# Performance work log

Hardware: AMD Instinct MI355X
Metric: run time of the kernel (lower is better)

Reference implementation:

```python
import jax, jax.numpy as jnp
import numpy as np

ALPHA = 2
SQUARE_LUT = jnp.arange(16, dtype=jnp.float32) ** 2
INV_SQRT_LUT = jnp.array([65535, 46341, 32768, 23170, 16384, 11585, 8192, 5793,
                          4096, 2896, 2048, 1448, 1024, 724, 512, 362], dtype=jnp.float32)


def setup_inputs() -> dict:
    key = jax.random.key(0)
    kx, = jax.random.split(key, 1)
    B, N = 8192, 4096
    x = jax.random.normal(kx, (B, N), dtype=jnp.float32)
    gamma = jnp.ones((N,), dtype=jnp.float32)
    beta = jnp.zeros((N,), dtype=jnp.float32)
    return {"x": x, "gamma": gamma, "beta": beta}


def _forward(x, gamma, beta):
    N = x.shape[1]
    # input quantization to int8 range (STE irrelevant for fwd)
    scale_in = jnp.max(jnp.abs(x)) / 127.0
    x_int = jnp.clip(jnp.round(x / scale_in), -127.0, 127.0)
    x_q = x_int * scale_in

    Ex = jnp.sum(x_q, axis=1, keepdims=True)

    abs_q = jnp.abs(x_q)
    top2 = jnp.floor(abs_q / 64.0)
    idx_h = jnp.clip(jnp.floor(abs_q / 16.0), 0, 15).astype(jnp.int32)
    idx_m = jnp.clip(jnp.mod(jnp.floor(abs_q / 2.0), 16.0), 0, 15).astype(jnp.int32)
    hi = top2 >= 1
    idx = jnp.where(hi, idx_h, idx_m)
    sq = SQUARE_LUT[idx]
    sq_decomp = jnp.where(hi, sq * 16.0, sq)
    sq_ref = sq_decomp * (2.0 ** (2 * ALPHA))
    Ex2 = jnp.sum(sq_ref, axis=1, keepdims=True)

    mu = Ex / N
    var = Ex2 / N - mu * mu
    var_int = jnp.clip(jnp.round(var), 1.0, 2.0 ** 16 - 1)
    msb = jnp.clip(jnp.floor(jnp.log2(var_int)), 0, 15).astype(jnp.int32)
    inv_std = INV_SQRT_LUT[msb] / (2.0 ** 16)

    x_norm = (x_q - mu) * inv_std
    y = x_norm * gamma + beta

    scale_out = jnp.max(jnp.abs(y)) / 127.0
    y_int = jnp.clip(jnp.round(y / scale_out), -127.0, 127.0)
    return y_int * scale_out


def reference(x, gamma, beta):
    return _forward(x, gamma, beta)
```

## Files before the change

### kernel.cpp

```cpp
#include <hip/hip_runtime.h>
#include <cstdint>
#include <cstddef>

#define NC    4096
#define NTHR  256
#define R4    4
#define NBUCK 256

typedef float v4f __attribute__((ext_vector_type(4)));

static __device__ __forceinline__ float waveReduceMax(float v) {
    #pragma unroll
    for (int off = 32; off > 0; off >>= 1)
        v = fmaxf(v, __shfl_down(v, off, 64));
    return v;
}
static __device__ __forceinline__ float waveReduceSum(float v) {
    #pragma unroll
    for (int off = 32; off > 0; off >>= 1)
        v += __shfl_down(v, off, 64);
    return v;
}

__device__ __forceinline__ float blockMax(float v, float* s4, int tid) {
    v = waveReduceMax(v);
    int lane = tid & 63, wid = tid >> 6;
    if (lane == 0) s4[wid] = v;
    __syncthreads();
    return fmaxf(fmaxf(s4[0], s4[1]), fmaxf(s4[2], s4[3]));
}

__device__ __forceinline__ void rowStatCompute(float Ex, float Ex2,
                                               float* mu_o, float* inv_o) {
    float mu  = Ex * (1.f / NC);
    float var = __fsub_rn(Ex2 * (1.f / NC), __fmul_rn(mu, mu));
    float var_f = fminf(fmaxf(rintf(var), 1.f), 65535.f);
    int vi = (int)var_f;
    int msb = min(31 - __clz(vi), 15);
    const float lut[16] = {65535.f, 46341.f, 32768.f, 23170.f, 16384.f, 11585.f,
                           8192.f, 5793.f, 4096.f, 2896.f, 2048.f, 1448.f,
                           1024.f, 724.f, 512.f, 362.f};
    *mu_o  = mu;
    *inv_o = lut[msb] * (1.f / 65536.f);
}

__global__ __launch_bounds__(NTHR) void k_absmax(const float* __restrict__ x,
                                                 unsigned int* __restrict__ amax_bits,
                                                 int n4) {
    const float4* x4 = (const float4*)x;
    int t = blockIdx.x * NTHR + threadIdx.x;
    int S = gridDim.x * NTHR;
    float m = 0.f;
    int full = (n4 / (S * 8)) * (S * 8);
    for (int base = t; base < full; base += S * 8) {
        float4 v[8];
        #pragma unroll
        for (int u = 0; u < 8; ++u) v[u] = x4[base + u * S];
        #pragma unroll
        for (int u = 0; u < 8; ++u)
            m = fmaxf(m, fmaxf(fmaxf(fabsf(v[u].x), fabsf(v[u].y)),
                               fmaxf(fabsf(v[u].z), fabsf(v[u].w))));
    }
    for (int i = full + t; i < n4; i += S) {
        float4 v = x4[i];
        m = fmaxf(m, fmaxf(fmaxf(fabsf(v.x), fabsf(v.y)),
                           fmaxf(fabsf(v.z), fabsf(v.w))));
    }
    __shared__ float s4[4];
    float b = blockMax(m, s4, threadIdx.x);
    if (threadIdx.x == 0) atomicMax(amax_bits, __float_as_uint(b));
}

__global__ __launch_bounds__(NTHR) void k_rowstats4(
    const float* __restrict__ x,
    const float* __restrict__ gamma,
    const float* __restrict__ beta,
    const unsigned int* __restrict__ amax_x_bits,
    unsigned int* __restrict__ ybuck,
    float2* __restrict__ row_stats,
    int* __restrict__ xi8)
{
    const int tid = threadIdx.x;
    const int base_row = blockIdx.x * R4;
    const float scale_in = __uint_as_float(*amax_x_bits) * (1.0f / 127.0f);
    const float r_in = 1.0f / scale_in;

    const float4* g4 = (const float4*)gamma;
    const float4* b4 = (const float4*)beta;
    float4 gh[4], bh[4];
    #pragma unroll
    for (int k = 0; k < 4; ++k) { gh[k] = g4[tid + k * NTHR]; bh[k] = b4[tid + k * NTHR]; }

    float exr[R4], ex2r[R4];
    int pack[R4][4];
    #pragma unroll
    for (int r = 0; r < R4; ++r) {
        const int row = base_row + r;
        const float4* xr = (const float4*)(x + (size_t)row * NC);
        float4 v[4];
        #pragma unroll
        for (int k = 0; k < 4; ++k) v[k] = xr[tid + k * NTHR];

        float ex = 0.f, ex2 = 0.f;
        #pragma unroll
        for (int k = 0; k < 4; ++k) {
            const float* pv = (const float*)&v[k];
            int pk = 0;
            #pragma unroll
            for (int j = 0; j < 4; ++j) {
                float xi = fminf(fmaxf(rintf(pv[j] * r_in), -127.f), 127.f);
                int ii = (int)xi;
                pk |= (ii & 255) << (8 * j);
                float q = xi * scale_in;
                ex += q;
                float aq = fabsf(q);
                bool hi = aq >= 64.f;
                int idx = hi ? min((int)(aq * 0.0625f), 15)
                             : (((int)(aq * 0.5f)) & 15);
                float sq = (float)(idx * idx);
                ex2 += hi ? sq * 256.f : sq * 16.f;
            }
            pack[r][k] = pk;
        }
        exr[r] = ex; ex2r[r] = ex2;
        int* wr = xi8 + (size_t)row * (NC / 4);
        #pragma unroll
        for (int k = 0; k < 4; ++k) wr[tid + k * NTHR] = pack[r][k];
    }

    #pragma unroll
    for (int r = 0; r < R4; ++r) {
        exr[r]  = waveReduceSum(exr[r]);
        ex2r[r] = waveReduceSum(ex2r[r]);
    }
    __shared__ float sred[4][8];
    __shared__ float2 s_st[R4];
    const int lane = tid & 63, wid = tid >> 6;
    if (lane == 0) {
        #pragma unroll
        for (int r = 0; r < R4; ++r) { sred[wid][r] = exr[r]; sred[wid][4 + r] = ex2r[r]; }
    }
    __syncthreads();
    if (tid < R4) {
        float Ex  = (sred[0][tid] + sred[1][tid]) + (sred[2][tid] + sred[3][tid]);
        float Ex2 = (sred[0][4 + tid] + sred[1][4 + tid]) + (sred[2][4 + tid] + sred[3][4 + tid]);
        float mu, inv;
        rowStatCompute(Ex, Ex2, &mu, &inv);
        s_st[tid] = make_float2(mu, inv);
        row_stats[base_row + tid] = make_float2(mu, inv);
    }
    __syncthreads();

    float ym = 0.f;
    #pragma unroll
    for (int r = 0; r < R4; ++r) {
        const float mu = s_st[r].x, inv = s_st[r].y;
        #pragma unroll
        for (int k = 0; k < 4; ++k) {
            const float* pg = (const float*)&gh[k];
            const float* pb = (const float*)&bh[k];
            int pk = pack[r][k];
            #pragma unroll
            for (int j = 0; j < 4; ++j) {
                int ii = (pk << (24 - 8 * j)) >> 24;
                float q = (float)ii * scale_in;
                float y = (q - mu) * inv * pg[j] + pb[j];
                ym = fmaxf(ym, fabsf(y));
            }
        }
    }
    __shared__ float smax[4];
    float bym = blockMax(ym, smax, tid);
    if (tid == 0) atomicMax(&ybuck[blockIdx.x & (NBUCK - 1)], __float_as_uint(bym));
}

__global__ __launch_bounds__(NTHR) void k_finalize4(
    const int* __restrict__ xi8,
    const float* __restrict__ gamma,
    const float* __restrict__ beta,
    const unsigned int* __restrict__ amax_x_bits,
    const unsigned int* __restrict__ ybuck,
    const float2* __restrict__ row_stats,
    float* __restrict__ out)
{
    const int tid = threadIdx.x;
    const int base_row = blockIdx.x * R4;
    const float scale_in = __uint_as_float(*amax_x_bits) * (1.0f / 127.0f);

    float by = __uint_as_float(ybuck[tid]);
    __shared__ float s4[4];
    float pym = blockMax(by, s4, tid);
    const float scale_out = pym * (1.f / 127.f);
    const float r_out = 1.f / scale_out;

    const float4* g4 = (const float4*)gamma;
    const float4* b4 = (const float4*)beta;
    float4 gh[4], bh[4];
    #pragma unroll
    for (int k = 0; k < 4; ++k) { gh[k] = g4[tid + k * NTHR]; bh[k] = b4[tid + k * NTHR]; }

    #pragma unroll
    for (int r = 0; r < R4; ++r) {
        const int row = base_row + r;
        const int* rd = xi8 + (size_t)row * (NC / 4);
        int pk[4];
        #pragma unroll
        for (int k = 0; k < 4; ++k) pk[k] = rd[tid + k * NTHR];
        const float2 st = row_stats[row];
        const float mu = st.x, inv = st.y;
        float* outr = out + (size_t)row * NC;
        #pragma unroll
        for (int k = 0; k < 4; ++k) {
            const float* pg = (const float*)&gh[k];
            const float* pb = (const float*)&bh[k];
            v4f o;
            #pragma unroll
            for (int j = 0; j < 4; ++j) {
                int ii = (pk[k] << (24 - 8 * j)) >> 24;
                float q = (float)ii * scale_in;
                float y = (q - mu) * inv * pg[j] + pb[j];
                float yi = fminf(fmaxf(rintf(y * r_out), -127.f), 127.f);
                o[j] = yi * scale_out;
            }
            __builtin_nontemporal_store(o, (v4f*)(outr + (tid + k * NTHR) * 4));
        }
    }
}

__global__ __launch_bounds__(256) void k_rowstats_fb(
    const float* __restrict__ x, const float* __restrict__ gamma,
    const float* __restrict__ beta, const unsigned int* __restrict__ amax_x_bits,
    unsigned int* __restrict__ amax_y_bits, float2* __restrict__ row_stats,
    int* __restrict__ xi8)
{
    const int row = blockIdx.x;
    const float scale_in = __uint_as_float(*amax_x_bits) * (1.0f / 127.0f);
    const float r_in = 1.0f / scale_in;
    const float4* xr = (const float4*)(x + (size_t)row * NC);
    const float4* g4 = (const float4*)gamma;
    const float4* b4 = (const float4*)beta;
    int pack[4];
    float ex = 0.f, ex2 = 0.f;
    #pragma unroll
    for (int k = 0; k < 4; ++k) {
        float4 v = xr[threadIdx.x + k * 256];
        const float* pv = (const float*)&v;
        int pk = 0;
        #pragma unroll
        for (int j = 0; j < 4; ++j) {
            float xi = fminf(fmaxf(rintf(pv[j] * r_in), -127.f), 127.f);
            int ii = (int)xi;
            pk |= (ii & 255) << (8 * j);
            float q = xi * scale_in;
            ex += q;
            float aq = fabsf(q);
            bool hi = aq >= 64.f;
            int idx = hi ? min((int)(aq * 0.0625f), 15) : (((int)(aq * 0.5f)) & 15);
            float sq = (float)(idx * idx);
            ex2 += hi ? sq * 256.f : sq * 16.f;
        }
        pack[k] = pk;
    }
    int* wr = xi8 + (size_t)row * (NC / 4);
    #pragma unroll
    for (int k = 0; k < 4; ++k) wr[threadIdx.x + k * 256] = pack[k];
    ex  = waveReduceSum(ex);
    ex2 = waveReduceSum(ex2);
    __shared__ float sred[8];
    __shared__ float sbc[2];
    int lane = threadIdx.x & 63, wid = threadIdx.x >> 6;
    if (lane == 0) { sred[wid] = ex; sred[4 + wid] = ex2; }
    __syncthreads();
    if (threadIdx.x == 0) {
        float Ex  = (sred[0] + sred[1]) + (sred[2] + sred[3]);
        float Ex2 = (sred[4] + sred[5]) + (sred[6] + sred[7]);
        float mu, inv;
        rowStatCompute(Ex, Ex2, &mu, &inv);
        sbc[0] = mu; sbc[1] = inv;
        row_stats[row] = make_float2(mu, inv);
    }
    __syncthreads();
    const float mu = sbc[0], inv = sbc[1];
    float ym = 0.f;
    #pragma unroll
    for (int k = 0; k < 4; ++k) {
        float4 g = g4[threadIdx.x + k * 256];
        float4 b = b4[threadIdx.x + k * 256];
        const float* pg = (const float*)&g;
        const float* pb = (const float*)&b;
        int pk = pack[k];
        #pragma unroll
        for (int j = 0; j < 4; ++j) {
            int ii = (pk << (24 - 8 * j)) >> 24;
            float q = (float)ii * scale_in;
            float y = (q - mu) * inv * pg[j] + pb[j];
            ym = fmaxf(ym, fabsf(y));
        }
    }
    __syncthreads();
    __shared__ float smax[4];
    float b = blockMax(ym, smax, threadIdx.x);
    if (threadIdx.x == 0) atomicMax(amax_y_bits, __float_as_uint(b));
}

__global__ __launch_bounds__(256) void k_finalize_fb(
    const int* __restrict__ xi8, const float* __restrict__ gamma,
    const float* __restrict__ beta, const unsigned int* __restrict__ amax_x_bits,
    const unsigned int* __restrict__ amax_y_bits,
    const float2* __restrict__ row_stats, float* __restrict__ out)
{
    const int row = blockIdx.x;
    const float scale_in  = __uint_as_float(*amax_x_bits) * (1.0f / 127.0f);
    const float scale_out = __uint_as_float(*amax_y_bits) * (1.0f / 127.0f);
    const float r_out = 1.0f / scale_out;
    const float2 st = row_stats[row];
    const float mu = st.x, inv = st.y;
    const int* xr = xi8 + (size_t)row * (NC / 4);
    float4* outr = (float4*)(out + (size_t)row * NC);
    const float4* g4 = (const float4*)gamma;
    const float4* b4 = (const float4*)beta;
    #pragma unroll
    for (int k = 0; k < 4; ++k) {
        int pk = xr[threadIdx.x + k * 256];
        float4 g = g4[threadIdx.x + k * 256];
        float4 b = b4[threadIdx.x + k * 256];
        float4 o;
        const float* pg = (const float*)&g;
        const float* pb = (const float*)&b;
        float* po = (float*)&o;
        #pragma unroll
        for (int j = 0; j < 4; ++j) {
            int ii = (pk << (24 - 8 * j)) >> 24;
            float q = (float)ii * scale_in;
            float y = (q - mu) * inv * pg[j] + pb[j];
            float yi = fminf(fmaxf(rintf(y * r_out), -127.f), 127.f);
            po[j] = yi * scale_out;
        }
        outr[threadIdx.x + k * 256] = o;
    }
}

extern "C" void kernel_launch(void* const* d_in, const int* in_sizes, int n_in,
                              void* d_out, int out_size, void* d_ws, size_t ws_size,
                              hipStream_t stream) {
    const float* x     = (const float*)d_in[0];
    const float* gamma = (const float*)d_in[1];
    const float* beta  = (const float*)d_in[2];
    float* out = (float*)d_out;

    const int n    = in_sizes[0];
    const int rows = n / NC;
    const int n4   = n / 4;

    unsigned int* amax_x = (unsigned int*)d_ws;
    unsigned int* amax_y = (unsigned int*)((char*)d_ws + 8);
    unsigned int* ybuck  = (unsigned int*)((char*)d_ws + 1024);
    float2* row_stats    = (float2*)((char*)d_ws + 4096);
    size_t i8_off = (4096 + (size_t)rows * 8 + 255) & ~(size_t)255;
    int* xi8 = (int*)((char*)d_ws + i8_off);
    bool ws_ok = (ws_size >= i8_off + (size_t)n);

    hipMemsetAsync(d_ws, 0, 4096, stream);

    k_absmax<<<512, NTHR, 0, stream>>>(x, amax_x, n4);

    if (ws_ok && (rows % R4) == 0) {
        k_rowstats4<<<rows / R4, NTHR, 0, stream>>>(x, gamma, beta, amax_x,
                                                    ybuck, row_stats, xi8);
        k_finalize4<<<rows / R4, NTHR, 0, stream>>>(xi8, gamma, beta, amax_x,
                                                    ybuck, row_stats, out);
    } else {
        k_rowstats_fb<<<rows, NTHR, 0, stream>>>(x, gamma, beta, amax_x, amax_y,
                                                 row_stats, xi8);
        k_finalize_fb<<<rows, NTHR, 0, stream>>>(xi8, gamma, beta, amax_x, amax_y,
                                                 row_stats, out);
    }
}
```

Measured before the change: 294.2 us.

## Map one wavefront per row in rowstats and finalize kernels

Row processing changes from a whole block sweeping four rows to one 64-lane wavefront per row. Row sums and the y-absmax are reduced with xor shuffles inside the wave, which removes the shared-memory stages and the __syncthreads barriers. Each lane now handles 16 float4 chunks and reloads gamma/beta per row instead of caching them across four rows. This adds register pressure and more gamma/beta loads, and issues one atomicMax per row instead of one per block.

```diff
diff --git a/kernel.cpp b/kernel.cpp
--- a/kernel.cpp
+++ b/kernel.cpp
@@ -4,7 +4,6 @@
 
 #define NC    4096
 #define NTHR  256
-#define R4    4
 #define NBUCK 256
 
 typedef float v4f __attribute__((ext_vector_type(4)));
@@ -13,12 +12,6 @@
     #pragma unroll
     for (int off = 32; off > 0; off >>= 1)
         v = fmaxf(v, __shfl_down(v, off, 64));
-    return v;
-}
-static __device__ __forceinline__ float waveReduceSum(float v) {
-    #pragma unroll
-    for (int off = 32; off > 0; off >>= 1)
-        v += __shfl_down(v, off, 64);
     return v;
 }
 
@@ -71,7 +64,7 @@
     if (threadIdx.x == 0) atomicMax(amax_bits, __float_as_uint(b));
 }
 
-__global__ __launch_bounds__(NTHR) void k_rowstats4(
+__global__ __launch_bounds__(NTHR) void k_rowstats_w(
     const float* __restrict__ x,
     const float* __restrict__ gamma,
     const float* __restrict__ beta,
@@ -80,31 +73,23 @@
     float2* __restrict__ row_stats,
     int* __restrict__ xi8)
 {
-    const int tid = threadIdx.x;
-    const int base_row = blockIdx.x * R4;
+    const int tid  = threadIdx.x;
+    const int lane = tid & 63;
+    const int row  = blockIdx.x * 4 + (tid >> 6);
     const float scale_in = __uint_as_float(*amax_x_bits) * (1.0f / 127.0f);
     const float r_in = 1.0f / scale_in;
 
-    const float4* g4 = (const float4*)gamma;
-    const float4* b4 = (const float4*)beta;
-    float4 gh[4], bh[4];
-    #pragma unroll
-    for (int k = 0; k < 4; ++k) { gh[k] = g4[tid + k * NTHR]; bh[k] = b4[tid + k * NTHR]; }
-
-    float exr[R4], ex2r[R4];
-    int pack[R4][4];
-    #pragma unroll
-    for (int r = 0; r < R4; ++r) {
-        const int row = base_row + r;
-        const float4* xr = (const float4*)(x + (size_t)row * NC);
-        float4 v[4];
-        #pragma unroll
-        for (int k = 0; k < 4; ++k) v[k] = xr[tid + k * NTHR];
-
-        float ex = 0.f, ex2 = 0.f;
-        #pragma unroll
-        for (int k = 0; k < 4; ++k) {
-            const float* pv = (const float*)&v[k];
+    const float4* xr = (const float4*)(x + (size_t)row * NC);
+    int pack[16];
+    float ex = 0.f, ex2 = 0.f;
+    #pragma unroll
+    for (int e = 0; e < 16; e += 8) {
+        float4 v[8];
+        #pragma unroll
+        for (int u = 0; u < 8; ++u) v[u] = xr[lane + 64 * (e + u)];
+        #pragma unroll
+        for (int u = 0; u < 8; ++u) {
+            const float* pv = (const float*)&v[u];
             int pk = 0;
             #pragma unroll
             for (int j = 0; j < 4; ++j) {
@@ -120,46 +105,41 @@
                 float sq = (float)(idx * idx);
                 ex2 += hi ? sq * 256.f : sq * 16.f;
             }
-            pack[r][k] = pk;
-        }
-        exr[r] = ex; ex2r[r] = ex2;
-        int* wr = xi8 + (size_t)row * (NC / 4);
-        #pragma unroll
-        for (int k = 0; k < 4; ++k) wr[tid + k * NTHR] = pack[r][k];
-    }
-
-    #pragma unroll
-    for (int r = 0; r < R4; ++r) {
-        exr[r]  = waveReduceSum(exr[r]);
-        ex2r[r] = waveReduceSum(ex2r[r]);
-    }
-    __shared__ float sred[4][8];
-    __shared__ float2 s_st[R4];
-    const int lane = tid & 63, wid = tid >> 6;
-    if (lane == 0) {
-        #pragma unroll
-        for (int r = 0; r < R4; ++r) { sred[wid][r] = exr[r]; sred[wid][4 + r] = ex2r[r]; }
-    }
-    __syncthreads();
-    if (tid < R4) {
-        float Ex  = (sred[0][tid] + sred[1][tid]) + (sred[2][tid] + sred[3][tid]);
-        float Ex2 = (sred[0][4 + tid] + sred[1][4 + tid]) + (sred[2][4 + tid] + sred[3][4 + tid]);
-        float mu, inv;
-        rowStatCompute(Ex, Ex2, &mu, &inv);
-        s_st[tid] = make_float2(mu, inv);
-        row_stats[base_row + tid] = make_float2(mu, inv);
-    }
-    __syncthreads();
-
+            pack[e + u] = pk;
+        }
+    }
+
+    int* wr = xi8 + (size_t)row * (NC / 4);
+    #pragma unroll
+    for (int e = 0; e < 16; ++e) wr[lane + 64 * e] = pack[e];
+
+    #pragma unroll
+    for (int off = 1; off < 64; off <<= 1) {
+        ex  += __shfl_xor(ex,  off, 64);
+        ex2 += __shfl_xor(ex2, off, 64);
+    }
+    ex  = __shfl(ex,  0, 64);
+    ex2 = __shfl(ex2, 0, 64);
+    float mu, inv;
+    rowStatCompute(ex, ex2, &mu, &inv);
+    if (lane == 0) row_stats[row] = make_float2(mu, inv);
+
+    const float4* g4 = (const float4*)gamma;
+    const float4* b4 = (const float4*)beta;
     float ym = 0.f;
     #pragma unroll
-    for (int r = 0; r < R4; ++r) {
-        const float mu = s_st[r].x, inv = s_st[r].y;
-        #pragma unroll
-        for (int k = 0; k < 4; ++k) {
-            const float* pg = (const float*)&gh[k];
-            const float* pb = (const float*)&bh[k];
-            int pk = pack[r][k];
+    for (int e = 0; e < 16; e += 4) {
+        float4 g[4], b[4];
+        #pragma unroll
+        for (int u = 0; u < 4; ++u) {
+            g[u] = g4[lane + 64 * (e + u)];
+            b[u] = b4[lane + 64 * (e + u)];
+        }
+        #pragma unroll
+        for (int u = 0; u < 4; ++u) {
+            const float* pg = (const float*)&g[u];
+            const float* pb = (const float*)&b[u];
+            int pk = pack[e + u];
             #pragma unroll
             for (int j = 0; j < 4; ++j) {
                 int ii = (pk << (24 - 8 * j)) >> 24;
@@ -169,12 +149,13 @@
             }
         }
     }
-    __shared__ float smax[4];
-    float bym = blockMax(ym, smax, tid);
-    if (tid == 0) atomicMax(&ybuck[blockIdx.x & (NBUCK - 1)], __float_as_uint(bym));
-}
-
-__global__ __launch_bounds__(NTHR) void k_finalize4(
+    #pragma unroll
+    for (int off = 1; off < 64; off <<= 1)
+        ym = fmaxf(ym, __shfl_xor(ym, off, 64));
+    if (lane == 0) atomicMax(&ybuck[row & (NBUCK - 1)], __float_as_uint(ym));
+}
+
+__global__ __launch_bounds__(NTHR) void k_finalize_w(
     const int* __restrict__ xi8,
     const float* __restrict__ gamma,
     const float* __restrict__ beta,
@@ -183,8 +164,9 @@
     const float2* __restrict__ row_stats,
     float* __restrict__ out)
 {
-    const int tid = threadIdx.x;
-    const int base_row = blockIdx.x * R4;
+    const int tid  = threadIdx.x;
+    const int lane = tid & 63;
+    const int row  = blockIdx.x * 4 + (tid >> 6);
     const float scale_in = __uint_as_float(*amax_x_bits) * (1.0f / 127.0f);
 
     float by = __uint_as_float(ybuck[tid]);
@@ -193,36 +175,37 @@
     const float scale_out = pym * (1.f / 127.f);
     const float r_out = 1.f / scale_out;
 
+    const float2 st = row_stats[row];
+    const float mu = st.x, inv = st.y;
+    const int* rd = xi8 + (size_t)row * (NC / 4);
+    float* outr = out + (size_t)row * NC;
     const float4* g4 = (const float4*)gamma;
     const float4* b4 = (const float4*)beta;
-    float4 gh[4], bh[4];
-    #pragma unroll
-    for (int k = 0; k < 4; ++k) { gh[k] = g4[tid + k * NTHR]; bh[k] = b4[tid + k * NTHR]; }
-
-    #pragma unroll
-    for (int r = 0; r < R4; ++r) {
-        const int row = base_row + r;
-        const int* rd = xi8 + (size_t)row * (NC / 4);
+
+    #pragma unroll
+    for (int e = 0; e < 16; e += 4) {
         int pk[4];
-        #pragma unroll
-        for (int k = 0; k < 4; ++k) pk[k] = rd[tid + k * NTHR];
-        const float2 st = row_stats[row];
-        const float mu = st.x, inv = st.y;
-        float* outr = out + (size_t)row * NC;
-        #pragma unroll
-        for (int k = 0; k < 4; ++k) {
-            const float* pg = (const float*)&gh[k];
-            const float* pb = (const float*)&bh[k];
+        float4 g[4], b[4];
+        #pragma unroll
+        for (int u = 0; u < 4; ++u) {
+            pk[u] = rd[lane + 64 * (e + u)];
+            g[u]  = g4[lane + 64 * (e + u)];
+            b[u]  = b4[lane + 64 * (e + u)];
+        }
+        #pragma unroll
+        for (int u = 0; u < 4; ++u) {
+            const float* pg = (const float*)&g[u];
+            const float* pb = (const float*)&b[u];
             v4f o;
             #pragma unroll
             for (int j = 0; j < 4; ++j) {
-                int ii = (pk[k] << (24 - 8 * j)) >> 24;
+                int ii = (pk[u] << (24 - 8 * j)) >> 24;
                 float q = (float)ii * scale_in;
                 float y = (q - mu) * inv * pg[j] + pb[j];
                 float yi = fminf(fmaxf(rintf(y * r_out), -127.f), 127.f);
                 o[j] = yi * scale_out;
             }
-            __builtin_nontemporal_store(o, (v4f*)(outr + (tid + k * NTHR) * 4));
+            __builtin_nontemporal_store(o, (v4f*)(outr + (lane + 64 * (e + u)) * 4));
         }
     }
 }
@@ -264,8 +247,11 @@
     int* wr = xi8 + (size_t)row * (NC / 4);
     #pragma unroll
     for (int k = 0; k < 4; ++k) wr[threadIdx.x + k * 256] = pack[k];
-    ex  = waveReduceSum(ex);
-    ex2 = waveReduceSum(ex2);
+    #pragma unroll
+    for (int off = 1; off < 64; off <<= 1) {
+        ex  += __shfl_xor(ex,  off, 64);
+        ex2 += __shfl_xor(ex2, off, 64);
+    }
     __shared__ float sred[8];
     __shared__ float sbc[2];
     int lane = threadIdx.x & 63, wid = threadIdx.x >> 6;
@@ -364,10 +350,10 @@
 
     k_absmax<<<512, NTHR, 0, stream>>>(x, amax_x, n4);
 
-    if (ws_ok && (rows % R4) == 0) {
-        k_rowstats4<<<rows / R4, NTHR, 0, stream>>>(x, gamma, beta, amax_x,
+    if (ws_ok && (rows % 4) == 0) {
+        k_rowstats_w<<<rows / 4, NTHR, 0, stream>>>(x, gamma, beta, amax_x,
                                                     ybuck, row_stats, xi8);
-        k_finalize4<<<rows / R4, NTHR, 0, stream>>>(xi8, gamma, beta, amax_x,
+        k_finalize_w<<<rows / 4, NTHR, 0, stream>>>(xi8, gamma, beta, amax_x,
                                                     ybuck, row_stats, out);
     } else {
         k_rowstats_fb<<<rows, NTHR, 0, stream>>>(x, gamma, beta, amax_x, amax_y,
```

Result: no change. 292.2 us (-0.7%).
